# Kernel optimization log

Measured on AMD Instinct MI355X. Metric: run time of the kernel, lower is better.

The kernel has to match this reference:

```python
import jax, jax.numpy as jnp
import numpy as np

KH, KW = 3, 3  # kernel size (stride 1, SAME padding, rate 1)


def extract_patches_same(x, kh, kw):
    """TF tf.image.extract_patches, stride 1, rate 1, SAME padding (zero pad).
    x: [B,H,W,C] -> [B,H,W,kh*kw,C], patch ordered (ki, kj) row-major like TF."""
    B, H, W, C = x.shape
    ph, pw = (kh - 1) // 2, (kw - 1) // 2  # TF SAME: pad_before = (k-1)//2 for stride 1
    xp = jnp.pad(x, ((0, 0), (ph, kh - 1 - ph), (pw, kw - 1 - pw), (0, 0)))
    patches = jnp.stack(
        [xp[:, i:i + H, j:j + W, :] for i in range(kh) for j in range(kw)], axis=3
    )
    return patches  # [B,H,W,P,C] with P = kh*kw


def max_times_plus_p4(x, kernel, times_kernel):
    """x: [B,H,W,Cin]; kernel, times_kernel: [kh,kw,Cin,F].
    out[b,r,i,j,f] = sum_c max_p (patch[b,i,j,p,c]*tK_rot[p,c,f] + K_rot[p,c,f])."""
    kh, kw = kernel.shape[0], kernel.shape[1]
    patches = extract_patches_same(x, kh, kw)  # [B,H,W,P,C]
    res = []
    for r in range(4):  # 4 P4 rotations of the structuring elements
        k_rot = jnp.rot90(kernel, k=r, axes=(0, 1)).reshape(kh * kw, kernel.shape[2], kernel.shape[3])
        t_rot = jnp.rot90(times_kernel, k=r, axes=(0, 1)).reshape(kh * kw, kernel.shape[2], kernel.shape[3])
        # tropical (max-times-plus) lifting: mult-add then max over patch, sum over channel
        z = patches[..., None] * t_rot + k_rot          # [B,H,W,P,C,F]
        res.append(jnp.sum(jnp.max(z, axis=3), axis=3))  # [B,H,W,F]
    return jnp.stack(res, axis=1)  # [B,4,H,W,F]


def setup_inputs() -> dict:
    key = jax.random.key(0)
    k1, k2, k3 = jax.random.split(key, 3)
    B, H, W, Cin, F = 4, 64, 64, 16, 32
    x = jax.random.normal(k1, (B, H, W, Cin), dtype=jnp.float32)
    kernel = jax.random.normal(k2, (KH, KW, Cin, F), dtype=jnp.float32)
    times_kernel = jax.random.uniform(k3, (KH, KW, Cin, F), dtype=jnp.float32)  # NonNeg constraint
    return {"x": x, "kernel": kernel, "times_kernel": times_kernel}


def reference(x, kernel, times_kernel):
    return max_times_plus_p4(x, kernel, times_kernel)
```

## Files before the change

### kernel.cpp

```cpp
#include <hip/hip_runtime.h>

#define B_  4
#define H_  64
#define W_  64
#define C_  16
#define F_  32

#define NWE (8 * 9 * F_)
#define NXE (3 * 34 * 4)

typedef _Float16 h2 __attribute__((ext_vector_type(2)));

__device__ __forceinline__ h2 pack2(float a, float b) {
    h2 r; r.x = (_Float16)a; r.y = (_Float16)b; return r;
}

__device__ __forceinline__ float acc_dot2(h2 m, float c) {
#if __has_builtin(__builtin_amdgcn_fdot2)
    h2 one; one.x = (_Float16)1.0f; one.y = (_Float16)1.0f;
    return __builtin_amdgcn_fdot2(m, one, c, false);
#else
    return c + (float)m.x + (float)m.y;
#endif
}

__global__ __launch_bounds__(256) void mtp_main(const float* __restrict__ x,
                                                const float* __restrict__ kern,
                                                const float* __restrict__ tker,
                                                float* __restrict__ out) {
    __shared__ h2 wlds[NWE * 2];
    __shared__ h2 xlds[3][34][8];

    const int tid  = threadIdx.x;
    const int bidx = blockIdx.x;
    const int half = bidx & 1;
    const int i    = (bidx >> 1) & 63;
    const int b    = bidx >> 7;

    #pragma unroll
    for (int e0 = 0; e0 < 9; ++e0) {
        int e   = e0 * 256 + tid;
        int f   = e & 31;
        int t   = e >> 5;
        int q   = t % 9;
        int ccp = t / 9;
        int s0 = (q * C_ + ccp * 2 + 0) * F_ + f;
        int s1 = (q * C_ + ccp * 2 + 1) * F_ + f;
        wlds[e * 2 + 0] = pack2(tker[s0], tker[s1]);
        wlds[e * 2 + 1] = pack2(kern[s0], kern[s1]);
    }
    for (int e = tid; e < NXE; e += 256) {
        int cc4 = e & 3;
        int t   = e >> 2;
        int cl  = t % 34;
        int di  = t / 34;
        int ro  = i + di - 1;
        int co  = half * 32 + cl - 1;
        float4 v = make_float4(0.f, 0.f, 0.f, 0.f);
        if (ro >= 0 && ro < H_ && co >= 0 && co < W_)
            v = *reinterpret_cast<const float4*>(
                    x + ((b * H_ + ro) * W_ + co) * C_ + cc4 * 4);
        xlds[di][cl][cc4 * 2 + 0] = pack2(v.x, v.y);
        xlds[di][cl][cc4 * 2 + 1] = pack2(v.z, v.w);
    }
    __syncthreads();

    const int lane = tid & 63;
    const int f    = lane & 31;
    const int ps   = lane >> 5;
    const int w    = tid >> 6;
    const int cb   = w * 8 + ps;

    float acc[4][4];
    #pragma unroll
    for (int it = 0; it < 4; ++it)
        #pragma unroll
        for (int r = 0; r < 4; ++r) acc[it][r] = 0.f;

    #pragma unroll 1
    for (int cc = 0; cc < 8; ++cc) {
        h2 wt[9], wk[9];
        #pragma unroll
        for (int q = 0; q < 9; ++q) {
            int bi = ((cc * 9 + q) * F_ + f) * 2;
            wt[q] = wlds[bi];
            wk[q] = wlds[bi + 1];
        }
        h2 xh[3][9];
        #pragma unroll
        for (int dr = 0; dr < 3; ++dr)
            #pragma unroll
            for (int lc = 0; lc < 9; ++lc)
                xh[dr][lc] = xlds[dr][cb + lc][cc];

        #pragma unroll
        for (int it = 0; it < 4; ++it) {
            #pragma unroll
            for (int r = 0; r < 4; ++r) {
                h2 z[9];
                #pragma unroll
                for (int q = 0; q < 9; ++q) {
                    const int a = q / 3, bq = q % 3;
                    int di, dj;
                    switch (r) {
                        case 0:  di = a;      dj = bq;     break;
                        case 1:  di = 2 - bq; dj = a;      break;
                        case 2:  di = 2 - a;  dj = 2 - bq; break;
                        default: di = bq;     dj = 2 - a;  break;
                    }
                    z[q] = xh[di][it * 2 + dj] * wt[q] + wk[q];
                }
                h2 m1 = __builtin_elementwise_max(__builtin_elementwise_max(z[0], z[1]), z[2]);
                h2 m2 = __builtin_elementwise_max(__builtin_elementwise_max(z[3], z[4]), z[5]);
                h2 m3 = __builtin_elementwise_max(__builtin_elementwise_max(z[6], z[7]), z[8]);
                h2 mm = __builtin_elementwise_max(__builtin_elementwise_max(m1, m2), m3);
                acc[it][r] = acc_dot2(mm, acc[it][r]);
            }
        }
    }

    const int jg = half * 32 + w * 8 + ps;
    #pragma unroll
    for (int r = 0; r < 4; ++r) {
        float* op = out + ((((b * 4 + r) * H_ + i) * W_ + jg) * F_ + f);
        #pragma unroll
        for (int it = 0; it < 4; ++it)
            op[it * 2 * F_] = acc[it][r];
    }
}

extern "C" void kernel_launch(void* const* d_in, const int* in_sizes, int n_in,
                              void* d_out, int out_size, void* d_ws, size_t ws_size,
                              hipStream_t stream) {
    const float* x    = (const float*)d_in[0];
    const float* kern = (const float*)d_in[1];
    const float* tker = (const float*)d_in[2];
    float* out = (float*)d_out;

    hipLaunchKernelGGL(mtp_main, dim3(B_ * H_ * 2), dim3(256), 0, stream,
                       x, kern, tker, out);
}
```

Before: 16.95 us.

## Repack LDS weights and inputs for 128-bit vector reads

Weights are repacked into float4 entries holding two taps' (tker, kern) fp16 pairs, so each thread fetches 9 taps with 5 vector LDS reads instead of 18 scalar ones. Input columns are stored channel-major in two copies, one shifted by one column, so each lane reads 16-byte-aligned float4 chunks whatever its column parity. The cc loop is also unrolled by 2 instead of 1. This cuts the number of LDS instructions and the address arithmetic, at the cost of extra LDS footprint, duplicated stores and more register pressure.

```diff
diff --git a/kernel.cpp b/kernel.cpp
--- a/kernel.cpp
+++ b/kernel.cpp
@@ -6,14 +6,13 @@
 #define C_  16
 #define F_  32
 
-#define NWE (8 * 9 * F_)
-#define NXE (3 * 34 * 4)
-
 typedef _Float16 h2 __attribute__((ext_vector_type(2)));
 
 __device__ __forceinline__ h2 pack2(float a, float b) {
     h2 r; r.x = (_Float16)a; r.y = (_Float16)b; return r;
 }
+__device__ __forceinline__ float h2f(h2 v) { return __builtin_bit_cast(float, v); }
+__device__ __forceinline__ h2 f2h(float v) { return __builtin_bit_cast(h2, v); }
 
 __device__ __forceinline__ float acc_dot2(h2 m, float c) {
 #if __has_builtin(__builtin_amdgcn_fdot2)
@@ -28,8 +27,9 @@
                                                 const float* __restrict__ kern,
                                                 const float* __restrict__ tker,
                                                 float* __restrict__ out) {
-    __shared__ h2 wlds[NWE * 2];
-    __shared__ h2 xlds[3][34][8];
+    __shared__ float4 wlds[8][5][32];
+    __shared__ float4 xa[3][8][9];
+    __shared__ float4 xb[3][8][9];
 
     const int tid  = threadIdx.x;
     const int bidx = blockIdx.x;
@@ -38,18 +38,29 @@
     const int b    = bidx >> 7;
 
     #pragma unroll
-    for (int e0 = 0; e0 < 9; ++e0) {
-        int e   = e0 * 256 + tid;
-        int f   = e & 31;
-        int t   = e >> 5;
-        int q   = t % 9;
-        int ccp = t / 9;
-        int s0 = (q * C_ + ccp * 2 + 0) * F_ + f;
-        int s1 = (q * C_ + ccp * 2 + 1) * F_ + f;
-        wlds[e * 2 + 0] = pack2(tker[s0], tker[s1]);
-        wlds[e * 2 + 1] = pack2(kern[s0], kern[s1]);
+    for (int e0 = 0; e0 < 5; ++e0) {
+        int e  = e0 * 256 + tid;
+        int f  = e & 31;
+        int t  = e >> 5;
+        int qp = t % 5;
+        int cc = t / 5;
+        int c0 = cc * 2, c1 = c0 + 1;
+        int q0 = qp * 2;
+        int q1 = (qp < 4) ? q0 + 1 : 8;
+        float4 v;
+        v.x = h2f(pack2(tker[(q0 * C_ + c0) * F_ + f], tker[(q0 * C_ + c1) * F_ + f]));
+        v.y = h2f(pack2(kern[(q0 * C_ + c0) * F_ + f], kern[(q0 * C_ + c1) * F_ + f]));
+        h2 zt = (qp < 4) ? pack2(tker[(q1 * C_ + c0) * F_ + f], tker[(q1 * C_ + c1) * F_ + f])
+                         : pack2(0.f, 0.f);
+        h2 zk = (qp < 4) ? pack2(kern[(q1 * C_ + c0) * F_ + f], kern[(q1 * C_ + c1) * F_ + f])
+                         : pack2(0.f, 0.f);
+        v.z = h2f(zt);
+        v.w = h2f(zk);
+        wlds[cc][qp][f] = v;
     }
-    for (int e = tid; e < NXE; e += 256) {
+    float* xaf = reinterpret_cast<float*>(xa);
+    float* xbf = reinterpret_cast<float*>(xb);
+    for (int e = tid; e < 3 * 34 * 4; e += 256) {
         int cc4 = e & 3;
         int t   = e >> 2;
         int cl  = t % 34;
@@ -60,8 +71,15 @@
         if (ro >= 0 && ro < H_ && co >= 0 && co < W_)
             v = *reinterpret_cast<const float4*>(
                     x + ((b * H_ + ro) * W_ + co) * C_ + cc4 * 4);
-        xlds[di][cl][cc4 * 2 + 0] = pack2(v.x, v.y);
-        xlds[di][cl][cc4 * 2 + 1] = pack2(v.z, v.w);
+        float p0 = h2f(pack2(v.x, v.y));
+        float p1 = h2f(pack2(v.z, v.w));
+        int cc0 = cc4 * 2, cc1 = cc0 + 1;
+        xaf[(di * 8 + cc0) * 36 + cl] = p0;
+        xaf[(di * 8 + cc1) * 36 + cl] = p1;
+        if (cl >= 1) {
+            xbf[(di * 8 + cc0) * 36 + cl - 1] = p0;
+            xbf[(di * 8 + cc1) * 36 + cl - 1] = p1;
+        }
     }
     __syncthreads();
 
@@ -69,7 +87,7 @@
     const int f    = lane & 31;
     const int ps   = lane >> 5;
     const int w    = tid >> 6;
-    const int cb   = w * 8 + ps;
+    const int w2   = w * 2;
 
     float acc[4][4];
     #pragma unroll
@@ -77,21 +95,33 @@
         #pragma unroll
         for (int r = 0; r < 4; ++r) acc[it][r] = 0.f;
 
-    #pragma unroll 1
+    const float4* xp0 = (ps ? &xb[0][0][0] : &xa[0][0][0]) + w2;
+
+    #pragma unroll 2
     for (int cc = 0; cc < 8; ++cc) {
+        float4 ws0 = wlds[cc][0][f];
+        float4 ws1 = wlds[cc][1][f];
+        float4 ws2 = wlds[cc][2][f];
+        float4 ws3 = wlds[cc][3][f];
+        float4 ws4 = wlds[cc][4][f];
         h2 wt[9], wk[9];
+        wt[0] = f2h(ws0.x); wk[0] = f2h(ws0.y); wt[1] = f2h(ws0.z); wk[1] = f2h(ws0.w);
+        wt[2] = f2h(ws1.x); wk[2] = f2h(ws1.y); wt[3] = f2h(ws1.z); wk[3] = f2h(ws1.w);
+        wt[4] = f2h(ws2.x); wk[4] = f2h(ws2.y); wt[5] = f2h(ws2.z); wk[5] = f2h(ws2.w);
+        wt[6] = f2h(ws3.x); wk[6] = f2h(ws3.y); wt[7] = f2h(ws3.z); wk[7] = f2h(ws3.w);
+        wt[8] = f2h(ws4.x); wk[8] = f2h(ws4.y);
+
+        const float4* xp = xp0 + cc * 9;
+        float xc[3][12];
         #pragma unroll
-        for (int q = 0; q < 9; ++q) {
-            int bi = ((cc * 9 + q) * F_ + f) * 2;
-            wt[q] = wlds[bi];
-            wk[q] = wlds[bi + 1];
+        for (int dr = 0; dr < 3; ++dr) {
+            float4 a = xp[dr * 72 + 0];
+            float4 bq4 = xp[dr * 72 + 1];
+            float4 c = xp[dr * 72 + 2];
+            xc[dr][0] = a.x;  xc[dr][1] = a.y;  xc[dr][2]  = a.z;  xc[dr][3]  = a.w;
+            xc[dr][4] = bq4.x; xc[dr][5] = bq4.y; xc[dr][6] = bq4.z; xc[dr][7] = bq4.w;
+            xc[dr][8] = c.x;  xc[dr][9] = c.y;  xc[dr][10] = c.z;  xc[dr][11] = c.w;
         }
-        h2 xh[3][9];
-        #pragma unroll
-        for (int dr = 0; dr < 3; ++dr)
-            #pragma unroll
-            for (int lc = 0; lc < 9; ++lc)
-                xh[dr][lc] = xlds[dr][cb + lc][cc];
 
         #pragma unroll
         for (int it = 0; it < 4; ++it) {
@@ -108,7 +138,7 @@
                         case 2:  di = 2 - a;  dj = 2 - bq; break;
                         default: di = bq;     dj = 2 - a;  break;
                     }
-                    z[q] = xh[di][it * 2 + dj] * wt[q] + wk[q];
+                    z[q] = f2h(xc[di][it * 2 + dj]) * wt[q] + wk[q];
                 }
                 h2 m1 = __builtin_elementwise_max(__builtin_elementwise_max(z[0], z[1]), z[2]);
                 h2 m2 = __builtin_elementwise_max(__builtin_elementwise_max(z[3], z[4]), z[5]);
```

Result: slower. 17.42 us (+2.8%).

## Pre-pack weights in separate kernel and split rows into quarter-width blocks

Applied to the files above, without the earlier changes.

Moves the fp16 packing of kernel and times_kernel into a small prep kernel that writes a global packed buffer, so each main block only does a straight float2 copy into LDS. The main kernel now splits each row into four 16-column segments, doubling the grid to 1024 blocks and halving per-thread work and the x halo tile. The intent is more parallelism and less per-block conversion work. In exchange it adds a second launch and a redundant 9 KB weight copy into LDS per block, with twice as many blocks doing that copy.

```diff
diff --git a/kernel.cpp b/kernel.cpp
--- a/kernel.cpp
+++ b/kernel.cpp
@@ -7,13 +7,13 @@
 #define F_  32
 
 #define NWE (8 * 9 * F_)
-#define NXE (3 * 34 * 4)
 
 typedef _Float16 h2 __attribute__((ext_vector_type(2)));
 
 __device__ __forceinline__ h2 pack2(float a, float b) {
     h2 r; r.x = (_Float16)a; r.y = (_Float16)b; return r;
 }
+__device__ __forceinline__ float h2f(h2 v) { return __builtin_bit_cast(float, v); }
 
 __device__ __forceinline__ float acc_dot2(h2 m, float c) {
 #if __has_builtin(__builtin_amdgcn_fdot2)
@@ -24,38 +24,49 @@
 #endif
 }
 
+__device__ h2 g_wpk[NWE * 2];
+
+__global__ void mtp_prep(const float* __restrict__ kern,
+                         const float* __restrict__ tker) {
+    int e = blockIdx.x * 256 + threadIdx.x;
+    if (e >= NWE) return;
+    int f   = e & 31;
+    int t   = e >> 5;
+    int q   = t % 9;
+    int ccp = t / 9;
+    int s0 = (q * C_ + ccp * 2) * F_ + f;
+    int s1 = s0 + F_;
+    h2 wt = pack2(tker[s0], tker[s1]);
+    h2 wk = pack2(kern[s0], kern[s1]);
+    *reinterpret_cast<float2*>(&g_wpk[e * 2]) = make_float2(h2f(wt), h2f(wk));
+}
+
 __global__ __launch_bounds__(256) void mtp_main(const float* __restrict__ x,
-                                                const float* __restrict__ kern,
-                                                const float* __restrict__ tker,
                                                 float* __restrict__ out) {
     __shared__ h2 wlds[NWE * 2];
-    __shared__ h2 xlds[3][34][8];
+    __shared__ h2 xlds[3][18][8];
 
     const int tid  = threadIdx.x;
     const int bidx = blockIdx.x;
-    const int half = bidx & 1;
-    const int i    = (bidx >> 1) & 63;
-    const int b    = bidx >> 7;
+    const int q4   = bidx & 3;
+    const int i    = (bidx >> 2) & 63;
+    const int b    = bidx >> 8;
+    const int jseg = q4 * 16;
 
-    #pragma unroll
-    for (int e0 = 0; e0 < 9; ++e0) {
-        int e   = e0 * 256 + tid;
-        int f   = e & 31;
-        int t   = e >> 5;
-        int q   = t % 9;
-        int ccp = t / 9;
-        int s0 = (q * C_ + ccp * 2 + 0) * F_ + f;
-        int s1 = (q * C_ + ccp * 2 + 1) * F_ + f;
-        wlds[e * 2 + 0] = pack2(tker[s0], tker[s1]);
-        wlds[e * 2 + 1] = pack2(kern[s0], kern[s1]);
+    {
+        const float2* src = reinterpret_cast<const float2*>(g_wpk);
+        float2* dst = reinterpret_cast<float2*>(wlds);
+        #pragma unroll
+        for (int e0 = 0; e0 < 9; ++e0)
+            dst[e0 * 256 + tid] = src[e0 * 256 + tid];
     }
-    for (int e = tid; e < NXE; e += 256) {
-        int cc4 = e & 3;
-        int t   = e >> 2;
-        int cl  = t % 34;
-        int di  = t / 34;
+    if (tid < 216) {
+        int cc4 = tid & 3;
+        int t   = tid >> 2;
+        int cl  = t % 18;
+        int di  = t / 18;
         int ro  = i + di - 1;
-        int co  = half * 32 + cl - 1;
+        int co  = jseg + cl - 1;
         float4 v = make_float4(0.f, 0.f, 0.f, 0.f);
         if (ro >= 0 && ro < H_ && co >= 0 && co < W_)
             v = *reinterpret_cast<const float4*>(
@@ -69,11 +80,11 @@
     const int f    = lane & 31;
     const int ps   = lane >> 5;
     const int w    = tid >> 6;
-    const int cb   = w * 8 + ps;
+    const int cb   = w * 4 + ps;
 
-    float acc[4][4];
+    float acc[2][4];
     #pragma unroll
-    for (int it = 0; it < 4; ++it)
+    for (int it = 0; it < 2; ++it)
         #pragma unroll
         for (int r = 0; r < 4; ++r) acc[it][r] = 0.f;
 
@@ -86,15 +97,15 @@
             wt[q] = wlds[bi];
             wk[q] = wlds[bi + 1];
         }
-        h2 xh[3][9];
+        h2 xh[3][5];
         #pragma unroll
         for (int dr = 0; dr < 3; ++dr)
             #pragma unroll
-            for (int lc = 0; lc < 9; ++lc)
+            for (int lc = 0; lc < 5; ++lc)
                 xh[dr][lc] = xlds[dr][cb + lc][cc];
 
         #pragma unroll
-        for (int it = 0; it < 4; ++it) {
+        for (int it = 0; it < 2; ++it) {
             #pragma unroll
             for (int r = 0; r < 4; ++r) {
                 h2 z[9];
@@ -119,12 +130,12 @@
         }
     }
 
-    const int jg = half * 32 + w * 8 + ps;
+    const int jg = jseg + w * 4 + ps;
     #pragma unroll
     for (int r = 0; r < 4; ++r) {
         float* op = out + ((((b * 4 + r) * H_ + i) * W_ + jg) * F_ + f);
         #pragma unroll
-        for (int it = 0; it < 4; ++it)
+        for (int it = 0; it < 2; ++it)
             op[it * 2 * F_] = acc[it][r];
     }
 }
@@ -137,6 +148,6 @@
     const float* tker = (const float*)d_in[2];
     float* out = (float*)d_out;
 
-    hipLaunchKernelGGL(mtp_main, dim3(B_ * H_ * 2), dim3(256), 0, stream,
-                       x, kern, tker, out);
+    hipLaunchKernelGGL(mtp_prep, dim3(9), dim3(256), 0, stream, kern, tker);
+    hipLaunchKernelGGL(mtp_main, dim3(B_ * H_ * 4), dim3(256), 0, stream, x, out);
 }
```

Result: slower. 21.91 us (+29.2%).
